# Kernel optimization log

Hardware: AMD Instinct MI355X
Metric: run time of the kernel (lower is better)

Reference implementation:

```python
import jax, jax.numpy as jnp
import numpy as np

ALPHA = 0.2  # LeakyReLU negative slope

def setup_inputs() -> dict:
    key = jax.random.key(0)
    k1, k2, k3 = jax.random.split(key, 3)
    B, N, IN_DIM = 16, 1024, 128
    HEADS, HEAD_DIM = 2, 64  # out_dim = 128
    h = jax.random.normal(k1, (B, N, IN_DIM), dtype=jnp.float32)
    # xavier_uniform with gain=1.414 ~ uniform(-b, b); exact init unimportant for correctness
    bW = 1.414 * np.sqrt(6.0 / (IN_DIM + HEAD_DIM))
    W = jax.random.uniform(k2, (HEADS, IN_DIM, HEAD_DIM), minval=-bW, maxval=bW, dtype=jnp.float32)
    ba = 1.414 * np.sqrt(6.0 / (2 * HEAD_DIM + 1))
    a = jax.random.uniform(k3, (HEADS, 2 * HEAD_DIM, 1), minval=-ba, maxval=ba, dtype=jnp.float32)
    return {"h": h, "W": W, "a": a}

def reference(h, W, a):
    B, N, in_dim = h.shape
    heads, _, head_dim = W.shape
    out_dim = heads * head_dim
    # h_prime: [B, N, H, D]
    hp = jnp.einsum('bni,hio->bnho', h, W)
    # Split additive attention: a . [h_i ; h_j] = a_src . h_i + a_dst . h_j (same math as concat)
    a_src = a[:, :head_dim, 0]   # [H, D]
    a_dst = a[:, head_dim:, 0]   # [H, D]
    e_src = jnp.einsum('bnhd,hd->bhn', hp, a_src)  # [B, H, N]
    e_dst = jnp.einsum('bmhd,hd->bhm', hp, a_dst)  # [B, H, N]
    e = e_src[:, :, :, None] + e_dst[:, :, None, :]  # [B, H, N, N]
    e = jnp.where(e >= 0, e, ALPHA * e)  # LeakyReLU(0.2)
    att = jax.nn.softmax(e, axis=-1)
    # dropout p=0.0 (eval-deterministic): no-op
    h_new = jnp.einsum('bhnm,bmho->bnho', att, hp).reshape(B, N, out_dim)
    out = h_new + h if in_dim == out_dim else h_new
    return jax.nn.elu(out)
```

## Files before the change

kernel.cpp:

```cpp
#include <hip/hip_runtime.h>
#include <math.h>


#define LOG2E 1.44269504088896340736f

typedef __bf16 bf16x8 __attribute__((ext_vector_type(8)));
typedef float floatx4 __attribute__((ext_vector_type(4)));

union U16x8 { uint4 u; bf16x8 b; };

__device__ __forceinline__ unsigned short f2bf(float f) {
    union { __bf16 b; unsigned short u; } x;
    x.b = (__bf16)f;
    return x.u;
}

__global__ __launch_bounds__(256) void gat_prep(
    const float* __restrict__ Wg,
    const float* __restrict__ ag,
    unsigned short* __restrict__ Wp,
    float* __restrict__ acat)
{
    const int t = threadIdx.x;
#pragma unroll
    for (int i = 0; i < 64; ++i) {
        int idx = i * 256 + t;
        int c = idx & 127, k = idx >> 7;
        float v = Wg[(c >> 6) * 8192 + k * 64 + (c & 63)];
        Wp[((k >> 3) * 128 + c) * 8 + (k & 7)] = f2bf(v);
    }
    if (t < 128) {
        acat[t]       = ag[(t >> 6) * 128 + (t & 63)];
        acat[128 + t] = ag[(t >> 6) * 128 + 64 + (t & 63)];
    }
}

__global__ __launch_bounds__(256) void gat_hp(
    const float* __restrict__ hg,
    const unsigned short* __restrict__ Wp,
    const float* __restrict__ acat,
    unsigned short* __restrict__ hpB,
    float* __restrict__ es_g,
    float* __restrict__ ed_g)
{
    const int t = threadIdx.x;
    const int lane = t & 63;
    const int wv = blockIdx.x * 4 + (t >> 6);
    const int rt = wv >> 1;
    const int half = wv & 1;
    const int n0 = rt * 16;
    const int col = lane & 15, quad = lane >> 4;

    floatx4 acc[4];
#pragma unroll
    for (int ct = 0; ct < 4; ++ct) acc[ct] = (floatx4){0.f, 0.f, 0.f, 0.f};

    const float* hrow = hg + (size_t)(n0 + col) * 128;
    const uint4* wp4 = (const uint4*)Wp;
#pragma unroll
    for (int kq = 0; kq < 4; ++kq) {
        float4 h0 = *(const float4*)(hrow + kq * 32 + quad * 8);
        float4 h1 = *(const float4*)(hrow + kq * 32 + quad * 8 + 4);
        bf16x8 af;
        af[0] = (__bf16)h0.x; af[1] = (__bf16)h0.y;
        af[2] = (__bf16)h0.z; af[3] = (__bf16)h0.w;
        af[4] = (__bf16)h1.x; af[5] = (__bf16)h1.y;
        af[6] = (__bf16)h1.z; af[7] = (__bf16)h1.w;
        const uint4* wbase = wp4 + (size_t)(kq * 4 + quad) * 128 + half * 64;
#pragma unroll
        for (int ct = 0; ct < 4; ++ct) {
            U16x8 bu; bu.u = wbase[ct * 16 + col];
            acc[ct] = __builtin_amdgcn_mfma_f32_16x16x32_bf16(af, bu.b, acc[ct], 0, 0, 0);
        }
    }

    const int b = n0 >> 10;
    const int nloc = n0 & 1023;
    const int bh = b * 2 + half;

    float esr[4] = {0.f, 0.f, 0.f, 0.f}, edr[4] = {0.f, 0.f, 0.f, 0.f};
#pragma unroll
    for (int ct = 0; ct < 4; ++ct) {
        int c = half * 64 + ct * 16 + col;
        float as = acat[c], ad = acat[128 + c];
#pragma unroll
        for (int r = 0; r < 4; ++r) {
            esr[r] = fmaf(acc[ct][r], as, esr[r]);
            edr[r] = fmaf(acc[ct][r], ad, edr[r]);
        }
    }
#pragma unroll
    for (int off = 1; off <= 8; off <<= 1) {
#pragma unroll
        for (int r = 0; r < 4; ++r) {
            esr[r] += __shfl_xor(esr[r], off, 64);
            edr[r] += __shfl_xor(edr[r], off, 64);
        }
    }
    if (col == 0) {
        size_t base = (size_t)bh * 1024 + nloc + quad * 4;
#pragma unroll
        for (int r = 0; r < 4; ++r) {
            es_g[base + r] = esr[r];
            ed_g[base + r] = edr[r];
        }
    }

    const int gloc = (nloc >> 3) + (quad >> 1);
#pragma unroll
    for (int ct = 0; ct < 4; ++ct) {
        int d = ct * 16 + col;
        uint2 pk;
        pk.x = (unsigned)f2bf(acc[ct][0]) | ((unsigned)f2bf(acc[ct][1]) << 16);
        pk.y = (unsigned)f2bf(acc[ct][2]) | ((unsigned)f2bf(acc[ct][3]) << 16);
        size_t idx = ((size_t)(bh * 128 + gloc) * 64 + d) * 8 + (quad & 1) * 4;
        *(uint2*)(hpB + idx) = pk;
    }
}

__global__ __launch_bounds__(256) void gat_attn(
    const float* __restrict__ hg,
    const unsigned short* __restrict__ hpB,
    const float* __restrict__ es_g,
    const float* __restrict__ ed_g,
    float* __restrict__ out)
{
    const int t = threadIdx.x;
    const int lane = t & 63;
    const int w = t >> 6;
    const int bh = blockIdx.x & 31;
    const int nt = blockIdx.x >> 5;
    const int b = bh >> 1, hh = bh & 1;
    const int rt = nt * 4 + w;
    const int n0 = rt * 16;
    const int col = lane & 15, quad = lane >> 4;

    const float* edrow = ed_g + (size_t)bh * 1024;

    float mx = -1e30f;
#pragma unroll
    for (int i = 0; i < 4; ++i) {
        float4 v = *(const float4*)(edrow + lane * 16 + i * 4);
        mx = fmaxf(mx, fmaxf(fmaxf(v.x, v.y), fmaxf(v.z, v.w)));
    }
#pragma unroll
    for (int off = 1; off < 64; off <<= 1) mx = fmaxf(mx, __shfl_xor(mx, off, 64));

    const float s2 = es_g[(size_t)bh * 1024 + n0 + col] * LOG2E;
    const float x0 = s2 + mx * LOG2E;
    const float M = fmaxf(x0, 0.2f * x0);
    const float s2m = s2 - M;
    const float s5m = 0.2f * s2 - M;
    const float K = LOG2E, K5 = 0.2f * LOG2E;

    floatx4 acc[4];
#pragma unroll
    for (int ct = 0; ct < 4; ++ct) acc[ct] = (floatx4){0.f, 0.f, 0.f, 0.f};
    float lsum = 0.f;

    const uint4* hb = (const uint4*)hpB + (size_t)bh * 8192;

    for (int m0 = 0; m0 < 1024; m0 += 32) {
        float4 d0 = *(const float4*)(edrow + m0 + quad * 8);
        float4 d1 = *(const float4*)(edrow + m0 + quad * 8 + 4);
        float dv[8] = {d0.x, d0.y, d0.z, d0.w, d1.x, d1.y, d1.z, d1.w};
        bf16x8 af;
#pragma unroll
        for (int j = 0; j < 8; ++j) {
            float a1 = fmaf(dv[j], K, s2m);
            float a2 = fmaf(dv[j], K5, s5m);
            float p = __builtin_amdgcn_exp2f(fmaxf(a1, a2));
            lsum += p;
            af[j] = (__bf16)p;
        }
        const int gm = (m0 >> 3) + quad;
#pragma unroll
        for (int ct = 0; ct < 4; ++ct) {
            U16x8 bu; bu.u = hb[gm * 64 + ct * 16 + col];
            acc[ct] = __builtin_amdgcn_mfma_f32_16x16x32_bf16(af, bu.b, acc[ct], 0, 0, 0);
        }
    }

    lsum += __shfl_xor(lsum, 16, 64);
    lsum += __shfl_xor(lsum, 32, 64);
    float inv[4];
#pragma unroll
    for (int r = 0; r < 4; ++r)
        inv[r] = __builtin_amdgcn_rcpf(__shfl(lsum, quad * 4 + r, 16));

#pragma unroll
    for (int ct = 0; ct < 4; ++ct) {
#pragma unroll
        for (int r = 0; r < 4; ++r) {
            int n = n0 + quad * 4 + r;
            size_t off = (size_t)(b * 1024 + n) * 128 + hh * 64 + ct * 16 + col;
            float v = acc[ct][r] * inv[r] + hg[off];
            out[off] = v > 0.f ? v : __builtin_amdgcn_exp2f(v * LOG2E) - 1.f;
        }
    }
}

extern "C" void kernel_launch(void* const* d_in, const int* in_sizes, int n_in,
                              void* d_out, int out_size, void* d_ws, size_t ws_size,
                              hipStream_t stream) {
    const float* h = (const float*)d_in[0];
    const float* W = (const float*)d_in[1];
    const float* a = (const float*)d_in[2];
    float* out = (float*)d_out;

    unsigned short* hpB = (unsigned short*)d_ws;
    float* es  = (float*)((char*)d_ws + (4u << 20));
    float* ed  = es + 32 * 1024;
    unsigned short* Wp = (unsigned short*)(ed + 32 * 1024);
    float* acat = (float*)((char*)Wp + 16384 * sizeof(unsigned short));

    gat_prep<<<1, 256, 0, stream>>>(W, a, Wp, acat);
    gat_hp<<<512, 256, 0, stream>>>(h, Wp, acat, hpB, es, ed);
    gat_attn<<<512, 256, 0, stream>>>(h, hpB, es, ed, out);
}
```

Measured before the change: 89.57 us.

## Split attention key range across waves with LDS reduction and prefetch loads

The attention kernel now gives each block a single 16-row tile and splits the 1024 keys across its four waves, each covering 256 keys. Partial accumulators and row sums are combined through shared memory, and each wave writes one 16-column slice of the output. The inner loop software-prefetches the next chunk of ed and hp values, and the prep kernel is spread across 16 blocks instead of one. This quadruples the grid to raise parallelism and shorten each wave's serial loop, at the cost of an LDS reduction, a barrier and redundant max/es computation per block.

```diff
diff --git a/kernel.cpp b/kernel.cpp
--- a/kernel.cpp
+++ b/kernel.cpp
@@ -22,14 +22,15 @@
     float* __restrict__ acat)
 {
     const int t = threadIdx.x;
-#pragma unroll
-    for (int i = 0; i < 64; ++i) {
-        int idx = i * 256 + t;
+    const int base = blockIdx.x * 1024;
+#pragma unroll
+    for (int i = 0; i < 4; ++i) {
+        int idx = base + i * 256 + t;
         int c = idx & 127, k = idx >> 7;
         float v = Wg[(c >> 6) * 8192 + k * 64 + (c & 63)];
         Wp[((k >> 3) * 128 + c) * 8 + (k & 7)] = f2bf(v);
     }
-    if (t < 128) {
+    if (blockIdx.x == 0 && t < 128) {
         acat[t]       = ag[(t >> 6) * 128 + (t & 63)];
         acat[128 + t] = ag[(t >> 6) * 128 + 64 + (t & 63)];
     }
@@ -118,21 +119,22 @@
     }
 }
 
-__global__ __launch_bounds__(256) void gat_attn(
+__global__ __launch_bounds__(256, 4) void gat_attn(
     const float* __restrict__ hg,
     const unsigned short* __restrict__ hpB,
     const float* __restrict__ es_g,
     const float* __restrict__ ed_g,
     float* __restrict__ out)
 {
+    __shared__ float red[4 * 64 * 17];
+
     const int t = threadIdx.x;
     const int lane = t & 63;
     const int w = t >> 6;
     const int bh = blockIdx.x & 31;
     const int nt = blockIdx.x >> 5;
     const int b = bh >> 1, hh = bh & 1;
-    const int rt = nt * 4 + w;
-    const int n0 = rt * 16;
+    const int n0 = nt * 16;
     const int col = lane & 15, quad = lane >> 4;
 
     const float* edrow = ed_g + (size_t)bh * 1024;
@@ -159,11 +161,31 @@
     float lsum = 0.f;
 
     const uint4* hb = (const uint4*)hpB + (size_t)bh * 8192;
-
-    for (int m0 = 0; m0 < 1024; m0 += 32) {
-        float4 d0 = *(const float4*)(edrow + m0 + quad * 8);
-        float4 d1 = *(const float4*)(edrow + m0 + quad * 8 + 4);
-        float dv[8] = {d0.x, d0.y, d0.z, d0.w, d1.x, d1.y, d1.z, d1.w};
+    const int mbase = w * 256;
+
+    float4 d0 = *(const float4*)(edrow + mbase + quad * 8);
+    float4 d1 = *(const float4*)(edrow + mbase + quad * 8 + 4);
+    int gm = (mbase >> 3) + quad;
+    uint4 bu0 = hb[gm * 64 + col];
+    uint4 bu1 = hb[gm * 64 + 16 + col];
+    uint4 bu2 = hb[gm * 64 + 32 + col];
+    uint4 bu3 = hb[gm * 64 + 48 + col];
+
+#pragma unroll
+    for (int i = 0; i < 8; ++i) {
+        float4 c0 = d0, c1 = d1;
+        uint4 cb0 = bu0, cb1 = bu1, cb2 = bu2, cb3 = bu3;
+        if (i < 7) {
+            int m1 = mbase + (i + 1) * 32;
+            d0 = *(const float4*)(edrow + m1 + quad * 8);
+            d1 = *(const float4*)(edrow + m1 + quad * 8 + 4);
+            gm = (m1 >> 3) + quad;
+            bu0 = hb[gm * 64 + col];
+            bu1 = hb[gm * 64 + 16 + col];
+            bu2 = hb[gm * 64 + 32 + col];
+            bu3 = hb[gm * 64 + 48 + col];
+        }
+        float dv[8] = {c0.x, c0.y, c0.z, c0.w, c1.x, c1.y, c1.z, c1.w};
         bf16x8 af;
 #pragma unroll
         for (int j = 0; j < 8; ++j) {
@@ -173,30 +195,47 @@
             lsum += p;
             af[j] = (__bf16)p;
         }
-        const int gm = (m0 >> 3) + quad;
-#pragma unroll
-        for (int ct = 0; ct < 4; ++ct) {
-            U16x8 bu; bu.u = hb[gm * 64 + ct * 16 + col];
-            acc[ct] = __builtin_amdgcn_mfma_f32_16x16x32_bf16(af, bu.b, acc[ct], 0, 0, 0);
-        }
+        U16x8 u0; u0.u = cb0;
+        U16x8 u1; u1.u = cb1;
+        U16x8 u2; u2.u = cb2;
+        U16x8 u3; u3.u = cb3;
+        acc[0] = __builtin_amdgcn_mfma_f32_16x16x32_bf16(af, u0.b, acc[0], 0, 0, 0);
+        acc[1] = __builtin_amdgcn_mfma_f32_16x16x32_bf16(af, u1.b, acc[1], 0, 0, 0);
+        acc[2] = __builtin_amdgcn_mfma_f32_16x16x32_bf16(af, u2.b, acc[2], 0, 0, 0);
+        acc[3] = __builtin_amdgcn_mfma_f32_16x16x32_bf16(af, u3.b, acc[3], 0, 0, 0);
     }
 
     lsum += __shfl_xor(lsum, 16, 64);
     lsum += __shfl_xor(lsum, 32, 64);
+
+    float* myred = red + (w * 64 + lane) * 17;
+#pragma unroll
+    for (int ct = 0; ct < 4; ++ct)
+#pragma unroll
+        for (int r = 0; r < 4; ++r) myred[ct * 4 + r] = acc[ct][r];
+    myred[16] = lsum;
+    __syncthreads();
+
+    float facc[4] = {0.f, 0.f, 0.f, 0.f};
+    float ltot = 0.f;
+#pragma unroll
+    for (int v = 0; v < 4; ++v) {
+        const float* rr = red + (v * 64 + lane) * 17;
+#pragma unroll
+        for (int r = 0; r < 4; ++r) facc[r] += rr[w * 4 + r];
+        ltot += rr[16];
+    }
     float inv[4];
 #pragma unroll
     for (int r = 0; r < 4; ++r)
-        inv[r] = __builtin_amdgcn_rcpf(__shfl(lsum, quad * 4 + r, 16));
-
-#pragma unroll
-    for (int ct = 0; ct < 4; ++ct) {
-#pragma unroll
-        for (int r = 0; r < 4; ++r) {
-            int n = n0 + quad * 4 + r;
-            size_t off = (size_t)(b * 1024 + n) * 128 + hh * 64 + ct * 16 + col;
-            float v = acc[ct][r] * inv[r] + hg[off];
-            out[off] = v > 0.f ? v : __builtin_amdgcn_exp2f(v * LOG2E) - 1.f;
-        }
+        inv[r] = __builtin_amdgcn_rcpf(__shfl(ltot, quad * 4 + r, 16));
+
+#pragma unroll
+    for (int r = 0; r < 4; ++r) {
+        int n = n0 + quad * 4 + r;
+        size_t off = (size_t)(b * 1024 + n) * 128 + hh * 64 + w * 16 + col;
+        float v = facc[r] * inv[r] + hg[off];
+        out[off] = v > 0.f ? v : __builtin_amdgcn_exp2f(v * LOG2E) - 1.f;
     }
 }
 
@@ -214,7 +253,7 @@
     unsigned short* Wp = (unsigned short*)(ed + 32 * 1024);
     float* acat = (float*)((char*)Wp + 16384 * sizeof(unsigned short));
 
-    gat_prep<<<1, 256, 0, stream>>>(W, a, Wp, acat);
+    gat_prep<<<16, 256, 0, stream>>>(W, a, Wp, acat);
     gat_hp<<<512, 256, 0, stream>>>(h, Wp, acat, hpB, es, ed);
-    gat_attn<<<512, 256, 0, stream>>>(h, hpB, es, ed, out);
-}
+    gat_attn<<<2048, 256, 0, stream>>>(h, hpB, es, ed, out);
+}
```

New measurement: 86.57 us. 3.4% less time.
